# Optimization experiments

Hardware: AMD Instinct MI355X
Metric: run time of the kernel (lower is better)

## Reference

```python
import jax, jax.numpy as jnp
import numpy as np

F_, H_, W_ = 6, 16, 28          # latent video grid (frames, height, width)
DIM, NH = 1536, 12
HD = DIM // NH                   # 128
L = F_ * H_ * W_                 # 2688 tokens
EPS = 1e-6
BLOCK = 3 * H_ * W_              # block_causal_size = 3*frame_height*frame_width


def setup_inputs() -> dict:
    key = jax.random.key(0)
    ks = jax.random.split(key, 8)
    def lin(k):
        return jax.random.normal(k, (DIM, DIM), jnp.float32) * 0.02
    x = jax.random.normal(ks[0], (1, L, DIM), jnp.float32)
    # RoPE freqs: unit-modulus complex numbers stored as [...,(re,im)]
    ang = jax.random.uniform(ks[1], (1024, HD // 2), jnp.float32, -np.pi, np.pi)
    freqs = jnp.stack([jnp.cos(ang), jnp.sin(ang)], axis=-1)  # [1024, 64, 2]
    return {
        'x': x,
        'seq_lens': jnp.array([L], jnp.int32),
        'grid_sizes': jnp.array([[F_, H_, W_]], jnp.int32),
        'freqs': freqs,
        'Wq': lin(ks[2]), 'bq': jnp.zeros((DIM,), jnp.float32),
        'Wk': lin(ks[3]), 'bk': jnp.zeros((DIM,), jnp.float32),
        'Wv': lin(ks[4]), 'bv': jnp.zeros((DIM,), jnp.float32),
        'Wo': lin(ks[5]), 'bo': jnp.zeros((DIM,), jnp.float32),
        'gq': jnp.ones((DIM,), jnp.float32),
        'gk': jnp.ones((DIM,), jnp.float32),
    }


def _rmsnorm(x, g):
    # WanRMSNorm: x * rsqrt(mean(x^2) + eps) * weight
    return x * jax.lax.rsqrt(jnp.mean(x * x, axis=-1, keepdims=True) + EPS) * g


def _rope_apply(x, F, H, W, freqs, start_frame=0):
    # x: [B, L, n, d]; freqs: [1024, d//2, 2] (re, im). Per-axis split [c0, c3, c3].
    B, Lx, n, d = x.shape
    c = d // 2
    c3 = c // 3
    c0 = c - 2 * c3
    f0 = freqs[start_frame:start_frame + F, :c0]      # [F, c0, 2]
    f1 = freqs[:H, c0:c0 + c3]                        # [H, c3, 2]
    f2 = freqs[:W, c0 + c3:]                          # [W, c3, 2]
    ff = jnp.concatenate([
        jnp.broadcast_to(f0[:, None, None], (F, H, W, c0, 2)),
        jnp.broadcast_to(f1[None, :, None], (F, H, W, c3, 2)),
        jnp.broadcast_to(f2[None, None, :], (F, H, W, c3, 2)),
    ], axis=3).reshape(Lx, 1, c, 2)                   # [L, 1, c, 2]
    xr = x.reshape(B, Lx, n, c, 2)
    xre, xim = xr[..., 0], xr[..., 1]
    fre, fim = ff[None, ..., 0], ff[None, ..., 1]     # broadcast over batch, heads
    ore = xre * fre - xim * fim
    oim = xre * fim + xim * fre
    return jnp.stack([ore, oim], axis=-1).reshape(B, Lx, n, d)


def reference(x, seq_lens, grid_sizes, freqs, Wq, bq, Wk, bk, Wv, bv, Wo, bo, gq, gk):
    b, s = x.shape[:2]
    F = int(grid_sizes[0, 0]); H = int(grid_sizes[0, 1]); W = int(grid_sizes[0, 2])
    q = _rmsnorm(x @ Wq + bq, gq).reshape(b, s, NH, HD)
    k = _rmsnorm(x @ Wk + bk, gk).reshape(b, s, NH, HD)
    v = (x @ Wv + bv).reshape(b, s, NH, HD)
    rq = _rope_apply(q, F, H, W, freqs)
    rk = _rope_apply(k, F, H, W, freqs)
    # block-causal attention: query attends to keys in same-or-earlier 3-frame block
    scores = jnp.einsum('bihd,bjhd->bhij', rq, rk) * (HD ** -0.5)
    blk = jnp.arange(s) // (3 * H * W)
    mask = blk[None, :] <= blk[:, None]               # [s, s]
    scores = jnp.where(mask[None, None], scores, -1e30)
    attn = jax.nn.softmax(scores, axis=-1)
    out = jnp.einsum('bhij,bjhd->bihd', attn, v).reshape(b, s, DIM)
    return out @ Wo + bo
```

## Files before the change

kernel.cpp:

```cpp
#include <hip/hip_runtime.h>

#define L_SEQ 2688
#define DIM   1536
#define NH    12
#define HD    128
#define BLK_TOK 1344
#define HW_   448
#define W_    28
#define NKIT  24

typedef unsigned short u16;
typedef unsigned int   u32;
typedef __attribute__((ext_vector_type(4))) float f32x4;
typedef __attribute__((ext_vector_type(16))) float f32x16;
typedef __attribute__((ext_vector_type(8))) short s16x8;
typedef __attribute__((ext_vector_type(2))) int i32x2;
typedef __attribute__((ext_vector_type(4))) u32 u32x4;

__device__ __forceinline__ u16 f2b(float f) {
    u32 u = __builtin_bit_cast(u32, f);
    return (u16)((u + 0x7FFFu + ((u >> 16) & 1u)) >> 16);
}
__device__ __forceinline__ float b2f(u16 b) {
    return __builtin_bit_cast(float, (u32)b << 16);
}
__device__ __forceinline__ u32 cvt_pk_bf16(float lo, float hi) {
    u32 r;
    asm("v_cvt_pk_bf16_f32 %0, %1, %2" : "=v"(r) : "v"(lo), "v"(hi));
    return r;
}

__global__ __launch_bounds__(256) void k_cvt_x(const float* __restrict__ x,
                                               u16* __restrict__ xb, int n4) {
    int i = blockIdx.x * 256 + threadIdx.x;
    int stride = gridDim.x * 256;
    for (; i < n4; i += stride) {
        float4 v = ((const float4*)x)[i];
        ushort4 o;
        o.x = f2b(v.x); o.y = f2b(v.y); o.z = f2b(v.z); o.w = f2b(v.w);
        ((ushort4*)xb)[i] = o;
    }
}

__global__ __launch_bounds__(256) void k_trans_w(const float* __restrict__ w0,
                                                 const float* __restrict__ w1,
                                                 const float* __restrict__ w2,
                                                 const float* __restrict__ w3,
                                                 u16* __restrict__ wt_all) {
    const float* w = blockIdx.z == 0 ? w0 : blockIdx.z == 1 ? w1 : blockIdx.z == 2 ? w2 : w3;
    u16* wt = wt_all + (size_t)blockIdx.z * DIM * DIM;
    __shared__ float t[64][65];
    const int k0 = blockIdx.y * 64, n0 = blockIdx.x * 64;
    const int c = threadIdx.x & 63, rg = threadIdx.x >> 6;
#pragma unroll
    for (int it = 0; it < 16; ++it) {
        int r = rg * 16 + it;
        t[r][c] = w[(size_t)(k0 + r) * DIM + n0 + c];
    }
    __syncthreads();
#pragma unroll
    for (int it = 0; it < 16; ++it) {
        int r = rg * 16 + it;
        wt[(size_t)(n0 + r) * DIM + k0 + c] = f2b(t[c][r]);
    }
}

template<int OUTF>
__global__ __launch_bounds__(256) void k_gemm(const u16* __restrict__ A,
                                              const u16* __restrict__ Bt_all,
                                              const float* __restrict__ b0,
                                              const float* __restrict__ b1,
                                              const float* __restrict__ b2,
                                              void* __restrict__ out_all) {
    const int NW = OUTF ? 252 : 756;
    const int qc = NW >> 3, rq = NW & 7;
    const int xcd = blockIdx.x & 7, idx = blockIdx.x >> 3;
    const int work = (xcd < rq) ? xcd * (qc + 1) + idx
                                : rq * (qc + 1) + (xcd - rq) * qc + idx;
    int z, bm, bn;
    if (OUTF) { z = 0; bm = work / 12; bn = work - bm * 12; }
    else      { z = work / 252; int rem = work - z * 252; bm = rem / 12; bn = rem - bm * 12; }

    const u16* Bt = Bt_all + (size_t)z * DIM * DIM;
    const float* bias = z == 0 ? b0 : z == 1 ? b1 : b2;

    __shared__ u16 lbuf[2][2][8192];
    const int tid = threadIdx.x, lane = tid & 63, wid = tid >> 6;
    const int wm = wid >> 1, wn = wid & 1;
    const int q31 = lane & 31, hi = lane >> 5;

    const int sr = tid >> 3, sc = tid & 7;
    const int scol = 8 * (sc ^ (sr & 7));
    const u16* aRow = A  + (size_t)(bm * 128 + sr) * DIM + scol;
    const u16* bRow = Bt + (size_t)(bn * 128 + sr) * DIM + scol;

#define GSTAGE(KT, BUF)                                                            \
    {                                                                              \
        _Pragma("unroll")                                                          \
        for (int i = 0; i < 4; ++i)                                                \
            __builtin_amdgcn_global_load_lds(                                      \
                (const __attribute__((address_space(1))) u32*)(aRow + (size_t)i * 32 * DIM + (KT) * 64), \
                (__attribute__((address_space(3))) u32*)((char*)&lbuf[BUF][0][0] + i * 4096 + tid * 16), \
                16, 0, 0);                                                         \
        _Pragma("unroll")                                                          \
        for (int i = 0; i < 4; ++i)                                                \
            __builtin_amdgcn_global_load_lds(                                      \
                (const __attribute__((address_space(1))) u32*)(bRow + (size_t)i * 32 * DIM + (KT) * 64), \
                (__attribute__((address_space(3))) u32*)((char*)&lbuf[BUF][1][0] + i * 4096 + tid * 16), \
                16, 0, 0);                                                         \
    }

    f32x16 acc[2][2] = {};

    GSTAGE(0, 0);
    __syncthreads();
    for (int kt = 0; kt < NKIT; ++kt) {
        if (kt < NKIT - 1) GSTAGE(kt + 1, (kt + 1) & 1);
        const char* bufA = (const char*)&lbuf[kt & 1][0][0];
        const char* bufB = (const char*)&lbuf[kt & 1][1][0];
        s16x8 af[2][4], bf[2][4];
#pragma unroll
        for (int f = 0; f < 2; ++f)
#pragma unroll
            for (int kk = 0; kk < 4; ++kk) {
                const int ra = wm * 64 + f * 32 + q31;
                const int rb = wn * 64 + f * 32 + q31;
                const int cg = kk * 2 + hi;
                af[f][kk] = *(const s16x8*)(bufA + ra * 128 + (((cg) ^ (q31 & 7)) << 4));
                bf[f][kk] = *(const s16x8*)(bufB + rb * 128 + (((cg) ^ (q31 & 7)) << 4));
            }
        __builtin_amdgcn_s_setprio(1);
#pragma unroll
        for (int kk = 0; kk < 4; ++kk)
#pragma unroll
            for (int fm = 0; fm < 2; ++fm)
#pragma unroll
                for (int fn = 0; fn < 2; ++fn)
                    acc[fm][fn] = __builtin_amdgcn_mfma_f32_32x32x16_bf16(af[fm][kk], bf[fn][kk], acc[fm][fn], 0, 0, 0);
        __builtin_amdgcn_s_setprio(0);
        __syncthreads();
    }

#pragma unroll
    for (int fn = 0; fn < 2; ++fn) {
        const int col = bn * 128 + wn * 64 + fn * 32 + q31;
        const float bv = bias[col];
#pragma unroll
        for (int fm = 0; fm < 2; ++fm) {
#pragma unroll
            for (int e = 0; e < 16; ++e) {
                const int row = bm * 128 + wm * 64 + fm * 32 + (e & 3) + 8 * (e >> 2) + 4 * hi;
                const float v = acc[fm][fn][e] + bv;
                if (OUTF)
                    ((float*)out_all)[(size_t)row * DIM + col] = v;
                else
                    ((u16*)out_all)[(size_t)z * L_SEQ * DIM + (size_t)row * DIM + col] = f2b(v);
            }
        }
    }
#undef GSTAGE
}

__global__ __launch_bounds__(256) void k_norm_rope(const u16* __restrict__ pre_all,
                                                   const float* __restrict__ gq,
                                                   const float* __restrict__ gk,
                                                   const float* __restrict__ freqs,
                                                   u16* __restrict__ qh,
                                                   u16* __restrict__ kh) {
    const int which = blockIdx.y;
    const u16* pre = pre_all + (size_t)which * L_SEQ * DIM;
    const float* g = which ? gk : gq;
    u16* outh = which ? kh : qh;

    const int i = blockIdx.x;
    const int t = threadIdx.x;
    const u32* prow = (const u32*)(pre + (size_t)i * DIM);

    float re[3], im[3];
    float ss = 0.f;
#pragma unroll
    for (int a = 0; a < 3; ++a) {
        u32 p = prow[t + a * 256];
        float x = b2f((u16)(p & 0xFFFFu)), y = b2f((u16)(p >> 16));
        re[a] = x; im[a] = y;
        ss += x * x + y * y;
    }
#pragma unroll
    for (int o = 32; o > 0; o >>= 1) ss += __shfl_down(ss, o, 64);
    __shared__ float sred[4];
    if ((t & 63) == 0) sred[t >> 6] = ss;
    __syncthreads();
    float rms = rsqrtf((sred[0] + sred[1] + sred[2] + sred[3]) * (1.0f / DIM) + 1e-6f);

    const int f = i / HW_;
    const int rem = i - f * HW_;
    const int hp = rem / W_;
    const int wp = rem - hp * W_;
#pragma unroll
    for (int a = 0; a < 3; ++a) {
        int j = t + a * 256;
        int h = j >> 6, pj = j & 63;
        float2 gg = ((const float2*)g)[j];
        float x = re[a] * rms * gg.x;
        float y = im[a] * rms * gg.y;
        int ridx = pj < 22 ? f : (pj < 43 ? hp : wp);
        float2 cs = ((const float2*)freqs)[ridx * 64 + pj];
        float ore = x * cs.x - y * cs.y;
        float oim = x * cs.y + y * cs.x;
        u32 o = (u32)f2b(ore) | ((u32)f2b(oim) << 16);
        ((u32*)outh)[(size_t)h * (L_SEQ * 64) + (size_t)i * 64 + pj] = o;
    }
}

__global__ __launch_bounds__(256) void k_vtrans(const u16* __restrict__ vpre,
                                                u16* __restrict__ vt) {
    const int i0 = blockIdx.x * 64, d0 = blockIdx.y * 64, h = blockIdx.z;
    __shared__ u16 t[64][68];
    const int c = threadIdx.x & 63, rg = threadIdx.x >> 6;
#pragma unroll
    for (int it = 0; it < 16; ++it) {
        int r = rg * 16 + it;
        t[r][c] = vpre[(size_t)(i0 + r) * DIM + h * HD + d0 + c];
    }
    __syncthreads();
#pragma unroll
    for (int it = 0; it < 16; ++it) {
        int r = rg * 16 + it;
        vt[(size_t)h * (HD * L_SEQ) + (size_t)(d0 + r) * L_SEQ + i0 + c] = t[c][r];
    }
}

__global__ __launch_bounds__(256, 2) void k_attn(const u16* __restrict__ qh,
                                                 const u16* __restrict__ kh,
                                                 const u16* __restrict__ vt,
                                                 u16* __restrict__ ob,
                                                 float* __restrict__ Opart,
                                                 float* __restrict__ mlp) {
    __shared__ char lsm[2][32768];

    const int flat = blockIdx.x;
    const int xcd = flat & 7, idx = flat >> 3;
    const int work = (xcd < 4) ? (xcd * 95 + idx) : (380 + (xcd - 4) * 94 + idx);
    const int head = work / 63;
    const int bx = work - head * 63;
    int qt, kv0, mode;
    if (bx < 21)      { qt = bx;      kv0 = 0;  mode = 0; }
    else if (bx < 42) { qt = bx;      kv0 = 0;  mode = 1; }
    else              { qt = bx - 21; kv0 = 21; mode = 2; }

    const int tid = threadIdx.x, lane = tid & 63, w = tid >> 6;
    const int pairI = w >> 1;
    const int qhalf = w & 1;
    const int q31 = lane & 31, hi = lane >> 5;
    const size_t hOff = (size_t)head * ((size_t)L_SEQ * HD);
    const u16* Kh = kh + hOff;
    const u16* Vh = vt + hOff;
    const int qrow0 = qt * 64 + qhalf * 32;

    s16x8 aq[8];
#pragma unroll
    for (int kk = 0; kk < 8; ++kk)
        aq[kk] = *(const s16x8*)&qh[hOff + (size_t)(qrow0 + q31) * HD + kk * 16 + hi * 8];

    const int rh = tid >> 4, ck = tid & 15;
    const int rv = tid >> 3, cv = tid & 7;
    const int koff = 8 * (ck ^ rh);
    const int voff = 8 * (cv ^ (rv & 7));

#define STAGE_TILE(TG, BUF)                                                       \
    {                                                                             \
        char* dst = lsm[BUF];                                                     \
        _Pragma("unroll")                                                         \
        for (int i = 0; i < 4; ++i) {                                             \
            const u16* src = Kh + (size_t)((TG) * 64 + i * 16 + rh) * HD + koff;  \
            __builtin_amdgcn_global_load_lds(                                     \
                (const __attribute__((address_space(1))) u32*)src,                \
                (__attribute__((address_space(3))) u32*)(dst + i * 4096 + tid * 16), 16, 0, 0); \
        }                                                                         \
        _Pragma("unroll")                                                         \
        for (int i = 0; i < 4; ++i) {                                             \
            const u16* src = Vh + (size_t)(i * 32 + rv) * L_SEQ + (TG) * 64 + voff; \
            __builtin_amdgcn_global_load_lds(                                     \
                (const __attribute__((address_space(1))) u32*)src,                \
                (__attribute__((address_space(3))) u32*)(dst + 16384 + i * 4096 + tid * 16), 16, 0, 0); \
        }                                                                         \
    }

    f32x16 acc[4] = {};
    float mrun = -1e30f, lrun = 0.f;
    const float sc2 = 0.12751739646917983f;
    const int krow = pairI * 32 + q31;

    STAGE_TILE(kv0, 0);
    __syncthreads();
    for (int t = 0; t < 21; ++t) {
        if (t < 20) STAGE_TILE(kv0 + t + 1, (t + 1) & 1);
        const char* slot = lsm[t & 1];

        f32x16 sv0 = {}, sv1 = {};
        __builtin_amdgcn_s_setprio(1);
#pragma unroll
        for (int kk = 0; kk < 4; ++kk) {
            int off0 = krow * 256 + ((kk * 32 + hi * 16) ^ ((q31 & 15) << 4));
            int off1 = krow * 256 + (((kk + 4) * 32 + hi * 16) ^ ((q31 & 15) << 4));
            s16x8 kf0 = *(const s16x8*)(slot + off0);
            s16x8 kf1 = *(const s16x8*)(slot + off1);
            sv0 = __builtin_amdgcn_mfma_f32_32x32x16_bf16(kf0, aq[kk], sv0, 0, 0, 0);
            sv1 = __builtin_amdgcn_mfma_f32_32x32x16_bf16(kf1, aq[kk + 4], sv1, 0, 0, 0);
        }
        __builtin_amdgcn_s_setprio(0);
        f32x16 sv;
#pragma unroll
        for (int e = 0; e < 16; ++e) sv[e] = sv0[e] + sv1[e];

        float m8[8];
#pragma unroll
        for (int e = 0; e < 8; ++e) m8[e] = fmaxf(sv[e], sv[e + 8]);
        float m4a = fmaxf(m8[0], m8[1]), m4b = fmaxf(m8[2], m8[3]);
        float m4c = fmaxf(m8[4], m8[5]), m4d = fmaxf(m8[6], m8[7]);
        float mx = fmaxf(fmaxf(m4a, m4b), fmaxf(m4c, m4d));
        mx = fmaxf(mx, __shfl_xor(mx, 32, 64));
        mx *= sc2;
        const int resc = (mx - mrun) > 11.5f;
        const float mm = resc ? mx : mrun;
        const float fac = resc ? __builtin_amdgcn_exp2f(mrun - mm) : 1.0f;
        mrun = mm;
#pragma unroll
        for (int e = 0; e < 16; ++e)
            sv[e] = __builtin_amdgcn_exp2f(sv[e] * sc2 - mm);
        float s8[8];
#pragma unroll
        for (int e = 0; e < 8; ++e) s8[e] = sv[e] + sv[e + 8];
        float s4a = s8[0] + s8[1], s4b = s8[2] + s8[3];
        float s4c = s8[4] + s8[5], s4d = s8[6] + s8[7];
        float sum = (s4a + s4b) + (s4c + s4d);
        sum += __shfl_xor(sum, 32, 64);
        lrun = lrun * fac + sum;
        if (__any(resc)) {
#pragma unroll
            for (int ds = 0; ds < 4; ++ds)
#pragma unroll
                for (int e = 0; e < 16; ++e) acc[ds][e] *= fac;
        }

        s16x8 pa[2];
#pragma unroll
        for (int hf = 0; hf < 2; ++hf) {
            u32 a0 = cvt_pk_bf16(sv[hf * 8 + 0], sv[hf * 8 + 1]);
            u32 a1 = cvt_pk_bf16(sv[hf * 8 + 2], sv[hf * 8 + 3]);
            u32 b0 = cvt_pk_bf16(sv[hf * 8 + 4], sv[hf * 8 + 5]);
            u32 b1 = cvt_pk_bf16(sv[hf * 8 + 6], sv[hf * 8 + 7]);
            i32x2 r0 = __builtin_amdgcn_permlane32_swap((int)a0, (int)b0, false, false);
            i32x2 r1 = __builtin_amdgcn_permlane32_swap((int)a1, (int)b1, false, false);
            u32x4 fw;
            fw.x = (u32)r0.x; fw.y = (u32)r1.x; fw.z = (u32)r0.y; fw.w = (u32)r1.y;
            pa[hf] = __builtin_bit_cast(s16x8, fw);
        }

        __builtin_amdgcn_s_setprio(1);
#pragma unroll
        for (int jstep = 0; jstep < 2; ++jstep)
#pragma unroll
            for (int ds = 0; ds < 4; ++ds) {
                int off = 16384 + (ds * 32 + q31) * 128 +
                          ((pairI * 64 + jstep * 32 + hi * 16) ^ ((q31 & 7) << 4));
                s16x8 vf = *(const s16x8*)(slot + off);
                acc[ds] = __builtin_amdgcn_mfma_f32_32x32x16_bf16(vf, pa[jstep], acc[ds], 0, 0, 0);
            }
        __builtin_amdgcn_s_setprio(0);
        __syncthreads();
    }

    float2* mlb = (float2*)(lsm[1]);
    char* accb = lsm[0];
    if (w >= 2) {
        char* base = accb + qhalf * 16384 + lane * 256;
#pragma unroll
        for (int ds = 0; ds < 4; ++ds)
#pragma unroll
            for (int g = 0; g < 4; ++g) {
                f32x4 v4;
#pragma unroll
                for (int e = 0; e < 4; ++e) v4[e] = acc[ds][g * 4 + e];
                *(f32x4*)(base + (((ds * 4 + g) * 16) ^ ((lane & 15) << 4))) = v4;
            }
        if (hi == 0) {
            float2 t2; t2.x = mrun; t2.y = lrun;
            mlb[qhalf * 32 + q31] = t2;
        }
    }
    __syncthreads();
    if (w < 2) {
        float2 ml2 = mlb[qhalf * 32 + q31];
        float M = fmaxf(mrun, ml2.x);
        float wa = exp2f(mrun - M), wb = exp2f(ml2.x - M);
        lrun = lrun * wa + ml2.y * wb;
        mrun = M;
        const char* base = accb + qhalf * 16384 + lane * 256;
#pragma unroll
        for (int ds = 0; ds < 4; ++ds)
#pragma unroll
            for (int g = 0; g < 4; ++g) {
                f32x4 v4 = *(const f32x4*)(base + (((ds * 4 + g) * 16) ^ ((lane & 15) << 4)));
#pragma unroll
                for (int e = 0; e < 4; ++e) acc[ds][g * 4 + e] = acc[ds][g * 4 + e] * wa + v4[e] * wb;
            }
        if (mode == 0) {
            const float inv = 1.0f / lrun;
            u16* orow = ob + (size_t)(qrow0 + q31) * DIM + head * HD;
#pragma unroll
            for (int ds = 0; ds < 4; ++ds)
#pragma unroll
                for (int g = 0; g < 4; ++g) {
                    uint2 pk2;
                    pk2.x = cvt_pk_bf16(acc[ds][g * 4 + 0] * inv, acc[ds][g * 4 + 1] * inv);
                    pk2.y = cvt_pk_bf16(acc[ds][g * 4 + 2] * inv, acc[ds][g * 4 + 3] * inv);
                    *(uint2*)(orow + ds * 32 + g * 8 + hi * 4) = pk2;
                }
        } else {
            const int pairo = (head * 21 + (qt - 21)) * 2 + (mode - 1);
            float* Op = Opart + (size_t)pairo * (64 * 128);
            const int rowl = qhalf * 32 + q31;
#pragma unroll
            for (int ds = 0; ds < 4; ++ds)
#pragma unroll
                for (int g = 0; g < 4; ++g) {
                    float4 v4;
                    v4.x = acc[ds][g * 4 + 0]; v4.y = acc[ds][g * 4 + 1];
                    v4.z = acc[ds][g * 4 + 2]; v4.w = acc[ds][g * 4 + 3];
                    *(float4*)(&Op[rowl * 128 + ds * 32 + g * 8 + hi * 4]) = v4;
                }
            if (hi == 0) {
                float2 t2; t2.x = mrun; t2.y = lrun;
                ((float2*)mlp)[(size_t)pairo * 64 + rowl] = t2;
            }
        }
    }
#undef STAGE_TILE
}

__global__ __launch_bounds__(256) void k_merge(const float* __restrict__ Opart,
                                               const float* __restrict__ mlp,
                                               u16* __restrict__ ob) {
    const int b = blockIdx.x;
    const int qt2 = b % 21, head = b / 21;
    const int pair = head * 21 + qt2;
    const float* O0 = Opart + (size_t)pair * 2 * 8192;
    const float* O1 = O0 + 8192;
    const int tid = threadIdx.x;
    const int row = tid >> 2, cs = (tid & 3) * 32;
    float2 a = ((const float2*)mlp)[(size_t)pair * 2 * 64 + row];
    float2 c = ((const float2*)mlp)[(size_t)(pair * 2 + 1) * 64 + row];
    float M = fmaxf(a.x, c.x);
    float w0 = exp2f(a.x - M), w1 = exp2f(c.x - M);
    float inv = 1.0f / (w0 * a.y + w1 * c.y);
    w0 *= inv; w1 *= inv;
    const int rowg = BLK_TOK + qt2 * 64 + row;
    u32* orow = (u32*)(ob + (size_t)rowg * DIM + head * HD + cs);
    const float4* p0 = (const float4*)(O0 + row * 128 + cs);
    const float4* p1 = (const float4*)(O1 + row * 128 + cs);
#pragma unroll
    for (int u = 0; u < 8; ++u) {
        float4 x0 = p0[u], x1 = p1[u];
        float o0 = x0.x * w0 + x1.x * w1;
        float o1 = x0.y * w0 + x1.y * w1;
        float o2 = x0.z * w0 + x1.z * w1;
        float o3 = x0.w * w0 + x1.w * w1;
        orow[u * 2]     = (u32)f2b(o0) | ((u32)f2b(o1) << 16);
        orow[u * 2 + 1] = (u32)f2b(o2) | ((u32)f2b(o3) << 16);
    }
}

extern "C" void kernel_launch(void* const* d_in, const int* in_sizes, int n_in,
                              void* d_out, int out_size, void* d_ws, size_t ws_size,
                              hipStream_t stream) {
    const float* x     = (const float*)d_in[0];
    const float* freqs = (const float*)d_in[3];
    const float* Wq    = (const float*)d_in[4];
    const float* bq    = (const float*)d_in[5];
    const float* Wk    = (const float*)d_in[6];
    const float* bk    = (const float*)d_in[7];
    const float* Wv    = (const float*)d_in[8];
    const float* bv    = (const float*)d_in[9];
    const float* Wo    = (const float*)d_in[10];
    const float* bo    = (const float*)d_in[11];
    const float* gq    = (const float*)d_in[12];
    const float* gk    = (const float*)d_in[13];

    const size_t LD = (size_t)L_SEQ * DIM;
    u16* wt_all  = (u16*)d_ws;
    u16* xb      = wt_all + (size_t)4 * DIM * DIM;
    u16* pre_all = xb + LD;
    u16* qh      = pre_all + 3 * LD;
    u16* kh2     = qh + LD;
    u16* vt      = kh2 + LD;
    u16* ob      = vt + LD;
    float* Opart = (float*)pre_all;
    float* mlp   = Opart + (size_t)12 * 21 * 2 * 64 * 128;

    k_cvt_x<<<2016, 256, 0, stream>>>(x, xb, (int)(LD / 4));
    k_trans_w<<<dim3(24, 24, 4), 256, 0, stream>>>(Wq, Wk, Wv, Wo, wt_all);
    k_gemm<0><<<dim3(756), 256, 0, stream>>>(xb, wt_all, bq, bk, bv, pre_all);
    k_norm_rope<<<dim3(L_SEQ, 2), 256, 0, stream>>>(pre_all, gq, gk, freqs, qh, kh2);
    k_vtrans<<<dim3(42, 2, NH), 256, 0, stream>>>(pre_all + 2 * LD, vt);
    k_attn<<<dim3(756), 256, 0, stream>>>(qh, kh2, vt, ob, Opart, mlp);
    k_merge<<<dim3(252), 256, 0, stream>>>(Opart, mlp, ob);
    k_gemm<1><<<dim3(252), 256, 0, stream>>>(ob, wt_all + (size_t)3 * DIM * DIM, bo, bo, bo, d_out);
}
```

Baseline: 160.4 us.

## Share each staged K/V tile across two query tiles with 512-thread attention blocks

Each attention block now has 8 waves covering two 64-row query tiles that use the same KV range. Every K/V tile staged into LDS is therefore used by both, which halves the K/V loads per query tile and the grid size (756 to 396 blocks). The cost is idle waves in the last block of each group, since 21 query tiles is odd. The larger block may also lower occupancy and adds more waves to every __syncthreads barrier.

New measurement: 171.0 us. 1.07x slower.

```diff
diff --git a/kernel.cpp b/kernel.cpp
--- a/kernel.cpp
+++ b/kernel.cpp
@@ -230,32 +230,39 @@
     }
 }
 
-__global__ __launch_bounds__(256, 2) void k_attn(const u16* __restrict__ qh,
+__global__ __launch_bounds__(512, 2) void k_attn(const u16* __restrict__ qh,
                                                  const u16* __restrict__ kh,
                                                  const u16* __restrict__ vt,
                                                  u16* __restrict__ ob,
                                                  float* __restrict__ Opart,
                                                  float* __restrict__ mlp) {
     __shared__ char lsm[2][32768];
+    __shared__ float2 mlb2[2][64];
 
     const int flat = blockIdx.x;
     const int xcd = flat & 7, idx = flat >> 3;
-    const int work = (xcd < 4) ? (xcd * 95 + idx) : (380 + (xcd - 4) * 94 + idx);
-    const int head = work / 63;
-    const int bx = work - head * 63;
-    int qt, kv0, mode;
-    if (bx < 21)      { qt = bx;      kv0 = 0;  mode = 0; }
-    else if (bx < 42) { qt = bx;      kv0 = 0;  mode = 1; }
-    else              { qt = bx - 21; kv0 = 21; mode = 2; }
+    const int work = (xcd < 4) ? (xcd * 50 + idx) : (200 + (xcd - 4) * 49 + idx);
+    const int head = work / 33;
+    const int rem = work - head * 33;
+    const int ctx = rem / 11, p = rem - (rem / 11) * 11;
+    const int qbase = (ctx == 0) ? 0 : 21;
+    const int kv0 = (ctx == 2) ? 21 : 0;
+    const int mode = ctx;
 
     const int tid = threadIdx.x, lane = tid & 63, w = tid >> 6;
-    const int pairI = w >> 1;
-    const int qhalf = w & 1;
+    const int slotS = w >> 2;
+    const int w2 = w & 3;
+    const int pairI = w2 >> 1;
+    const int qhalf = w2 & 1;
     const int q31 = lane & 31, hi = lane >> 5;
+    const int qt = qbase + 2 * p + slotS;
+    const bool qvalid = (2 * p + slotS) < 21;
+    const int qtc = qvalid ? qt : qbase;
+
     const size_t hOff = (size_t)head * ((size_t)L_SEQ * HD);
     const u16* Kh = kh + hOff;
     const u16* Vh = vt + hOff;
-    const int qrow0 = qt * 64 + qhalf * 32;
+    const int qrow0 = qtc * 64 + qhalf * 32;
 
     s16x8 aq[8];
 #pragma unroll
@@ -264,25 +271,25 @@
 
     const int rh = tid >> 4, ck = tid & 15;
     const int rv = tid >> 3, cv = tid & 7;
-    const int koff = 8 * (ck ^ rh);
+    const int koff = 8 * (ck ^ (rh & 15));
     const int voff = 8 * (cv ^ (rv & 7));
 
 #define STAGE_TILE(TG, BUF)                                                       \
     {                                                                             \
         char* dst = lsm[BUF];                                                     \
         _Pragma("unroll")                                                         \
-        for (int i = 0; i < 4; ++i) {                                             \
-            const u16* src = Kh + (size_t)((TG) * 64 + i * 16 + rh) * HD + koff;  \
+        for (int i = 0; i < 2; ++i) {                                             \
+            const u16* src = Kh + (size_t)((TG) * 64 + i * 32 + rh) * HD + koff;  \
             __builtin_amdgcn_global_load_lds(                                     \
                 (const __attribute__((address_space(1))) u32*)src,                \
-                (__attribute__((address_space(3))) u32*)(dst + i * 4096 + tid * 16), 16, 0, 0); \
+                (__attribute__((address_space(3))) u32*)(dst + i * 8192 + tid * 16), 16, 0, 0); \
         }                                                                         \
         _Pragma("unroll")                                                         \
-        for (int i = 0; i < 4; ++i) {                                             \
-            const u16* src = Vh + (size_t)(i * 32 + rv) * L_SEQ + (TG) * 64 + voff; \
+        for (int i = 0; i < 2; ++i) {                                             \
+            const u16* src = Vh + (size_t)(i * 64 + rv) * L_SEQ + (TG) * 64 + voff; \
             __builtin_amdgcn_global_load_lds(                                     \
                 (const __attribute__((address_space(1))) u32*)src,                \
-                (__attribute__((address_space(3))) u32*)(dst + 16384 + i * 4096 + tid * 16), 16, 0, 0); \
+                (__attribute__((address_space(3))) u32*)(dst + 16384 + i * 8192 + tid * 16), 16, 0, 0); \
         }                                                                         \
     }
 
@@ -297,84 +304,84 @@
         if (t < 20) STAGE_TILE(kv0 + t + 1, (t + 1) & 1);
         const char* slot = lsm[t & 1];
 
-        f32x16 sv0 = {}, sv1 = {};
-        __builtin_amdgcn_s_setprio(1);
-#pragma unroll
-        for (int kk = 0; kk < 4; ++kk) {
-            int off0 = krow * 256 + ((kk * 32 + hi * 16) ^ ((q31 & 15) << 4));
-            int off1 = krow * 256 + (((kk + 4) * 32 + hi * 16) ^ ((q31 & 15) << 4));
-            s16x8 kf0 = *(const s16x8*)(slot + off0);
-            s16x8 kf1 = *(const s16x8*)(slot + off1);
-            sv0 = __builtin_amdgcn_mfma_f32_32x32x16_bf16(kf0, aq[kk], sv0, 0, 0, 0);
-            sv1 = __builtin_amdgcn_mfma_f32_32x32x16_bf16(kf1, aq[kk + 4], sv1, 0, 0, 0);
+        if (qvalid) {
+            f32x16 sv0 = {}, sv1 = {};
+            __builtin_amdgcn_s_setprio(1);
+#pragma unroll
+            for (int kk = 0; kk < 4; ++kk) {
+                int off0 = krow * 256 + ((kk * 32 + hi * 16) ^ ((q31 & 15) << 4));
+                int off1 = krow * 256 + (((kk + 4) * 32 + hi * 16) ^ ((q31 & 15) << 4));
+                s16x8 kf0 = *(const s16x8*)(slot + off0);
+                s16x8 kf1 = *(const s16x8*)(slot + off1);
+                sv0 = __builtin_amdgcn_mfma_f32_32x32x16_bf16(kf0, aq[kk], sv0, 0, 0, 0);
+                sv1 = __builtin_amdgcn_mfma_f32_32x32x16_bf16(kf1, aq[kk + 4], sv1, 0, 0, 0);
+            }
+            __builtin_amdgcn_s_setprio(0);
+            f32x16 sv;
+#pragma unroll
+            for (int e = 0; e < 16; ++e) sv[e] = sv0[e] + sv1[e];
+
+            float m8[8];
+#pragma unroll
+            for (int e = 0; e < 8; ++e) m8[e] = fmaxf(sv[e], sv[e + 8]);
+            float m4a = fmaxf(m8[0], m8[1]), m4b = fmaxf(m8[2], m8[3]);
+            float m4c = fmaxf(m8[4], m8[5]), m4d = fmaxf(m8[6], m8[7]);
+            float mx = fmaxf(fmaxf(m4a, m4b), fmaxf(m4c, m4d));
+            mx = fmaxf(mx, __shfl_xor(mx, 32, 64));
+            mx *= sc2;
+            const int resc = (mx - mrun) > 11.5f;
+            const float mm = resc ? mx : mrun;
+            const float fac = resc ? __builtin_amdgcn_exp2f(mrun - mm) : 1.0f;
+            mrun = mm;
+#pragma unroll
+            for (int e = 0; e < 16; ++e)
+                sv[e] = __builtin_amdgcn_exp2f(sv[e] * sc2 - mm);
+            float s8[8];
+#pragma unroll
+            for (int e = 0; e < 8; ++e) s8[e] = sv[e] + sv[e + 8];
+            float s4a = s8[0] + s8[1], s4b = s8[2] + s8[3];
+            float s4c = s8[4] + s8[5], s4d = s8[6] + s8[7];
+            float sum = (s4a + s4b) + (s4c + s4d);
+            sum += __shfl_xor(sum, 32, 64);
+            lrun = lrun * fac + sum;
+            if (__any(resc)) {
+#pragma unroll
+                for (int ds = 0; ds < 4; ++ds)
+#pragma unroll
+                    for (int e = 0; e < 16; ++e) acc[ds][e] *= fac;
+            }
+
+            s16x8 pa[2];
+#pragma unroll
+            for (int hf = 0; hf < 2; ++hf) {
+                u32 a0 = cvt_pk_bf16(sv[hf * 8 + 0], sv[hf * 8 + 1]);
+                u32 a1 = cvt_pk_bf16(sv[hf * 8 + 2], sv[hf * 8 + 3]);
+                u32 b0 = cvt_pk_bf16(sv[hf * 8 + 4], sv[hf * 8 + 5]);
+                u32 b1 = cvt_pk_bf16(sv[hf * 8 + 6], sv[hf * 8 + 7]);
+                i32x2 r0 = __builtin_amdgcn_permlane32_swap((int)a0, (int)b0, false, false);
+                i32x2 r1 = __builtin_amdgcn_permlane32_swap((int)a1, (int)b1, false, false);
+                u32x4 fw;
+                fw.x = (u32)r0.x; fw.y = (u32)r1.x; fw.z = (u32)r0.y; fw.w = (u32)r1.y;
+                pa[hf] = __builtin_bit_cast(s16x8, fw);
+            }
+
+            __builtin_amdgcn_s_setprio(1);
+#pragma unroll
+            for (int jstep = 0; jstep < 2; ++jstep)
+#pragma unroll
+                for (int ds = 0; ds < 4; ++ds) {
+                    int off = 16384 + (ds * 32 + q31) * 128 +
+                              ((pairI * 64 + jstep * 32 + hi * 16) ^ ((q31 & 7) << 4));
+                    s16x8 vf = *(const s16x8*)(slot + off);
+                    acc[ds] = __builtin_amdgcn_mfma_f32_32x32x16_bf16(vf, pa[jstep], acc[ds], 0, 0, 0);
+                }
+            __builtin_amdgcn_s_setprio(0);
         }
-        __builtin_amdgcn_s_setprio(0);
-        f32x16 sv;
-#pragma unroll
-        for (int e = 0; e < 16; ++e) sv[e] = sv0[e] + sv1[e];
-
-        float m8[8];
-#pragma unroll
-        for (int e = 0; e < 8; ++e) m8[e] = fmaxf(sv[e], sv[e + 8]);
-        float m4a = fmaxf(m8[0], m8[1]), m4b = fmaxf(m8[2], m8[3]);
-        float m4c = fmaxf(m8[4], m8[5]), m4d = fmaxf(m8[6], m8[7]);
-        float mx = fmaxf(fmaxf(m4a, m4b), fmaxf(m4c, m4d));
-        mx = fmaxf(mx, __shfl_xor(mx, 32, 64));
-        mx *= sc2;
-        const int resc = (mx - mrun) > 11.5f;
-        const float mm = resc ? mx : mrun;
-        const float fac = resc ? __builtin_amdgcn_exp2f(mrun - mm) : 1.0f;
-        mrun = mm;
-#pragma unroll
-        for (int e = 0; e < 16; ++e)
-            sv[e] = __builtin_amdgcn_exp2f(sv[e] * sc2 - mm);
-        float s8[8];
-#pragma unroll
-        for (int e = 0; e < 8; ++e) s8[e] = sv[e] + sv[e + 8];
-        float s4a = s8[0] + s8[1], s4b = s8[2] + s8[3];
-        float s4c = s8[4] + s8[5], s4d = s8[6] + s8[7];
-        float sum = (s4a + s4b) + (s4c + s4d);
-        sum += __shfl_xor(sum, 32, 64);
-        lrun = lrun * fac + sum;
-        if (__any(resc)) {
-#pragma unroll
-            for (int ds = 0; ds < 4; ++ds)
-#pragma unroll
-                for (int e = 0; e < 16; ++e) acc[ds][e] *= fac;
-        }
-
-        s16x8 pa[2];
-#pragma unroll
-        for (int hf = 0; hf < 2; ++hf) {
-            u32 a0 = cvt_pk_bf16(sv[hf * 8 + 0], sv[hf * 8 + 1]);
-            u32 a1 = cvt_pk_bf16(sv[hf * 8 + 2], sv[hf * 8 + 3]);
-            u32 b0 = cvt_pk_bf16(sv[hf * 8 + 4], sv[hf * 8 + 5]);
-            u32 b1 = cvt_pk_bf16(sv[hf * 8 + 6], sv[hf * 8 + 7]);
-            i32x2 r0 = __builtin_amdgcn_permlane32_swap((int)a0, (int)b0, false, false);
-            i32x2 r1 = __builtin_amdgcn_permlane32_swap((int)a1, (int)b1, false, false);
-            u32x4 fw;
-            fw.x = (u32)r0.x; fw.y = (u32)r1.x; fw.z = (u32)r0.y; fw.w = (u32)r1.y;
-            pa[hf] = __builtin_bit_cast(s16x8, fw);
-        }
-
-        __builtin_amdgcn_s_setprio(1);
-#pragma unroll
-        for (int jstep = 0; jstep < 2; ++jstep)
-#pragma unroll
-            for (int ds = 0; ds < 4; ++ds) {
-                int off = 16384 + (ds * 32 + q31) * 128 +
-                          ((pairI * 64 + jstep * 32 + hi * 16) ^ ((q31 & 7) << 4));
-                s16x8 vf = *(const s16x8*)(slot + off);
-                acc[ds] = __builtin_amdgcn_mfma_f32_32x32x16_bf16(vf, pa[jstep], acc[ds], 0, 0, 0);
-            }
-        __builtin_amdgcn_s_setprio(0);
         __syncthreads();
     }
 
-    float2* mlb = (float2*)(lsm[1]);
-    char* accb = lsm[0];
-    if (w >= 2) {
-        char* base = accb + qhalf * 16384 + lane * 256;
+    if (pairI == 1 && qvalid) {
+        char* base = lsm[slotS] + qhalf * 16384 + lane * 256;
 #pragma unroll
         for (int ds = 0; ds < 4; ++ds)
 #pragma unroll
@@ -386,17 +393,17 @@
             }
         if (hi == 0) {
             float2 t2; t2.x = mrun; t2.y = lrun;
-            mlb[qhalf * 32 + q31] = t2;
+            mlb2[slotS][qhalf * 32 + q31] = t2;
         }
     }
     __syncthreads();
-    if (w < 2) {
-        float2 ml2 = mlb[qhalf * 32 + q31];
+    if (pairI == 0 && qvalid) {
+        float2 ml2 = mlb2[slotS][qhalf * 32 + q31];
         float M = fmaxf(mrun, ml2.x);
         float wa = exp2f(mrun - M), wb = exp2f(ml2.x - M);
         lrun = lrun * wa + ml2.y * wb;
         mrun = M;
-        const char* base = accb + qhalf * 16384 + lane * 256;
+        const char* base = lsm[slotS] + qhalf * 16384 + lane * 256;
 #pragma unroll
         for (int ds = 0; ds < 4; ++ds)
 #pragma unroll
@@ -503,7 +510,7 @@
     k_gemm<0><<<dim3(756), 256, 0, stream>>>(xb, wt_all, bq, bk, bv, pre_all);
     k_norm_rope<<<dim3(L_SEQ, 2), 256, 0, stream>>>(pre_all, gq, gk, freqs, qh, kh2);
     k_vtrans<<<dim3(42, 2, NH), 256, 0, stream>>>(pre_all + 2 * LD, vt);
-    k_attn<<<dim3(756), 256, 0, stream>>>(qh, kh2, vt, ob, Opart, mlp);
+    k_attn<<<dim3(396), 512, 0, stream>>>(qh, kh2, vt, ob, Opart, mlp);
     k_merge<<<dim3(252), 256, 0, stream>>>(Opart, mlp, ob);
     k_gemm<1><<<dim3(252), 256, 0, stream>>>(ob, wt_all + (size_t)3 * DIM * DIM, bo, bo, bo, d_out);
 }
```
